# Performance work log

Measured on AMD Instinct MI355X. Metric: run time of the kernel, lower is better.

The kernel has to match this reference:

```python
import jax, jax.numpy as jnp
import numpy as np

N_NODES = 50000
N_EDGES = 800000
IN_DIM = 256
OUT_DIM = 32
HEADS = 4
NEG_SLOPE = 0.2  # PyG GATConv default
LN_EPS = 1e-5


def setup_inputs() -> dict:
    key = jax.random.key(0)
    ks = jax.random.split(key, 8)
    x = jax.random.normal(ks[0], (N_NODES, IN_DIM), dtype=jnp.float32)
    edge_index = jax.random.randint(ks[1], (2, N_EDGES), 0, N_NODES, dtype=jnp.int64)
    # Glorot-ish scaling for stability
    W = jax.random.normal(ks[2], (IN_DIM, HEADS * OUT_DIM), dtype=jnp.float32) / np.sqrt(IN_DIM)
    att_src = jax.random.normal(ks[3], (HEADS, OUT_DIM), dtype=jnp.float32) / np.sqrt(OUT_DIM)
    att_dst = jax.random.normal(ks[4], (HEADS, OUT_DIM), dtype=jnp.float32) / np.sqrt(OUT_DIM)
    bias = jax.random.normal(ks[5], (HEADS * OUT_DIM,), dtype=jnp.float32) * 0.02
    gamma = jnp.ones((HEADS * OUT_DIM,), dtype=jnp.float32)
    beta = jnp.zeros((HEADS * OUT_DIM,), dtype=jnp.float32)
    return {"x": x, "edge_index": edge_index, "W": W, "att_src": att_src,
            "att_dst": att_dst, "bias": bias, "gamma": gamma, "beta": beta}


def reference(x, edge_index, W, att_src, att_dst, bias, gamma, beta):
    N = x.shape[0]
    H, C = att_src.shape
    # --- GATConv (PyG semantics, eval mode so attention dropout is identity) ---
    # add self-loops (PyG default add_self_loops=True)
    loops = jnp.arange(N, dtype=edge_index.dtype)
    src = jnp.concatenate([edge_index[0], loops])  # [E+N]
    dst = jnp.concatenate([edge_index[1], loops])
    h = (x @ W).reshape(N, H, C)                    # [N,H,C] (lin has no bias)
    a_s = jnp.einsum('nhc,hc->nh', h, att_src)      # [N,H]
    a_d = jnp.einsum('nhc,hc->nh', h, att_dst)
    e = jax.nn.leaky_relu(a_s[src] + a_d[dst], NEG_SLOPE)  # [E+N,H]
    # segment softmax over incoming edges of each destination node
    emax = jax.ops.segment_max(e, dst, num_segments=N)     # every node has a self-loop
    ee = jnp.exp(e - emax[dst])
    denom = jax.ops.segment_sum(ee, dst, num_segments=N)
    alpha = ee / denom[dst]                                 # [E+N,H]
    msg = h[src] * alpha[:, :, None]                        # [E+N,H,C]
    out = jax.ops.segment_sum(msg, dst, num_segments=N).reshape(N, H * C) + bias
    # --- LayerNorm ---
    mu = out.mean(-1, keepdims=True)
    var = ((out - mu) ** 2).mean(-1, keepdims=True)
    out = (out - mu) * jax.lax.rsqrt(var + LN_EPS) * gamma + beta
    # --- dropout (eval: identity) + ELU ---
    return jax.nn.elu(out)
```

## Files before the change

kernel.cpp:

```cpp
#include <hip/hip_runtime.h>
#include <hip/hip_bf16.h>
#include <cstdint>
#include <cstddef>

#define N_NODES 50000
#define N_EDGES 800000
#define IN_DIM 256
#define HC 128
#define HEADS 4
#define NEG_SLOPE 0.2f
#define LN_EPS 1e-5f

#define POISON_I ((int)0xAAAAAAAAu)

#define NSB ((N_NODES + 255) / 256)

typedef _Float16 f16x8 __attribute__((ext_vector_type(8)));
typedef _Float16 f16x2 __attribute__((ext_vector_type(2)));
typedef float f32x4 __attribute__((ext_vector_type(4)));

__device__ __forceinline__ float lrelu(float x) { return x > 0.f ? x : NEG_SLOPE * x; }
__device__ __forceinline__ unsigned pack_h2(float a, float b) {
    f16x2 h; h[0] = (_Float16)a; h[1] = (_Float16)b;
    return *(unsigned*)&h;
}

__global__ __launch_bounds__(256) void k_histW(
    const int* __restrict__ ei, const float* __restrict__ W,
    _Float16* __restrict__ W16, int* __restrict__ counts,
    int* __restrict__ rank)
{
    int b = blockIdx.x;
    if (b < 16) {
        int c = b * 256 + threadIdx.x;
        int col = c & 15, quad = (c >> 4) & 3, nt = (c >> 6) & 7, kt = c >> 9;
        int n = nt * 16 + col;
        f16x8 v;
#pragma unroll
        for (int j = 0; j < 8; ++j) {
            int k = kt * 32 + quad * 8 + j;
            v[j] = (_Float16)W[k * HC + n];
        }
        *(f16x8*)(W16 + (size_t)c * 8) = v;
    } else {
        int e = (b - 16) * 256 + threadIdx.x;
        if (e < N_EDGES)
            rank[e] = atomicAdd(&counts[ei[N_EDGES + e]], 1) - POISON_I;
    }
}

__global__ __launch_bounds__(256) void k1_mfma(
    const float* __restrict__ x, const _Float16* __restrict__ W16,
    const float* __restrict__ att_src, const float* __restrict__ att_dst,
    _Float16* __restrict__ h16, float* __restrict__ a_s, float* __restrict__ a_d)
{
    __shared__ _Float16 Wlds[32768];
    const int tid = threadIdx.x;

    {
        const uint4* g4 = (const uint4*)W16;
        uint4* s4 = (uint4*)Wlds;
#pragma unroll
        for (int it = 0; it < 16; ++it) s4[it * 256 + tid] = g4[it * 256 + tid];
    }

    const int wave = tid >> 6;
    const int lane = tid & 63;
    const int col  = lane & 15;
    const int quad = lane >> 4;
    const int m0   = blockIdx.x * 64 + wave * 16;

    const int rowA = min(m0 + col, N_NODES - 1);
    const float* xrow = x + (size_t)rowA * IN_DIM + quad * 8;

    float4 xr[16];
#pragma unroll
    for (int kt = 0; kt < 8; ++kt) {
        xr[2 * kt]     = *(const float4*)(xrow + kt * 32);
        xr[2 * kt + 1] = *(const float4*)(xrow + kt * 32 + 4);
    }
    __syncthreads();

    f32x4 acc[8];
#pragma unroll
    for (int nt = 0; nt < 8; ++nt) acc[nt] = (f32x4){0.f, 0.f, 0.f, 0.f};

#pragma unroll
    for (int kt = 0; kt < 8; ++kt) {
        float4 xa = xr[2 * kt], xb = xr[2 * kt + 1];
        f16x8 a;
        a[0] = (_Float16)xa.x; a[1] = (_Float16)xa.y;
        a[2] = (_Float16)xa.z; a[3] = (_Float16)xa.w;
        a[4] = (_Float16)xb.x; a[5] = (_Float16)xb.y;
        a[6] = (_Float16)xb.z; a[7] = (_Float16)xb.w;
#pragma unroll
        for (int nt = 0; nt < 8; ++nt) {
            f16x8 b = *(const f16x8*)&Wlds[((kt * 8 + nt) * 64 + quad * 16 + col) * 8];
            acc[nt] = __builtin_amdgcn_mfma_f32_16x16x32_f16(a, b, acc[nt], 0, 0, 0);
        }
    }

    f16x2* h2g = (f16x2*)h16;
#pragma unroll
    for (int a2 = 0; a2 < 4; ++a2) {
#pragma unroll
        for (int r = 0; r < 4; ++r) {
            int row = m0 + quad * 4 + r;
            if (row < N_NODES) {
                f16x2 hv;
                hv[0] = (_Float16)acc[2 * a2][r];
                hv[1] = (_Float16)acc[2 * a2 + 1][r];
                h2g[(size_t)row * 64 + a2 * 16 + col] = hv;
            }
        }
    }

    float pS[4][4], pD[4][4];
#pragma unroll
    for (int hd = 0; hd < 4; ++hd)
#pragma unroll
        for (int r = 0; r < 4; ++r) { pS[hd][r] = 0.f; pD[hd][r] = 0.f; }

#pragma unroll
    for (int nt = 0; nt < 8; ++nt) {
        int ch = nt * 16 + col;
        float sv = att_src[ch], dv = att_dst[ch];
        int hd = nt >> 1;
#pragma unroll
        for (int r = 0; r < 4; ++r) {
            pS[hd][r] += acc[nt][r] * sv;
            pD[hd][r] += acc[nt][r] * dv;
        }
    }
#pragma unroll
    for (int off = 1; off < 16; off <<= 1) {
#pragma unroll
        for (int hd = 0; hd < 4; ++hd)
#pragma unroll
            for (int r = 0; r < 4; ++r) {
                pS[hd][r] += __shfl_xor(pS[hd][r], off, 16);
                pD[hd][r] += __shfl_xor(pD[hd][r], off, 16);
            }
    }
    if (col == 0) {
#pragma unroll
        for (int r = 0; r < 4; ++r) {
            int row = m0 + quad * 4 + r;
            if (row < N_NODES) {
#pragma unroll
                for (int hd = 0; hd < 4; ++hd) {
                    a_s[row * HEADS + hd] = pS[hd][r];
                    a_d[row * HEADS + hd] = pD[hd][r];
                }
            }
        }
    }
}

__global__ __launch_bounds__(256) void k_scan1(const int* __restrict__ counts,
                                               int* __restrict__ starts,
                                               int* __restrict__ bsum) {
    __shared__ int s[256];
    int i = blockIdx.x * 256 + threadIdx.x;
    int v = (i < N_NODES) ? (counts[i] - POISON_I) : 0;
    s[threadIdx.x] = v; __syncthreads();
#pragma unroll
    for (int off = 1; off < 256; off <<= 1) {
        int t = (threadIdx.x >= off) ? s[threadIdx.x - off] : 0;
        __syncthreads();
        s[threadIdx.x] += t;
        __syncthreads();
    }
    if (i < N_NODES) starts[i] = s[threadIdx.x] - v;
    if (threadIdx.x == 255) bsum[blockIdx.x] = s[255];
}
__global__ __launch_bounds__(256) void k_scan2(int* __restrict__ bsum, int nb) {
    __shared__ int s[256];
    int v = (threadIdx.x < nb) ? bsum[threadIdx.x] : 0;
    s[threadIdx.x] = v; __syncthreads();
#pragma unroll
    for (int off = 1; off < 256; off <<= 1) {
        int t = (threadIdx.x >= off) ? s[threadIdx.x - off] : 0;
        __syncthreads();
        s[threadIdx.x] += t;
        __syncthreads();
    }
    if (threadIdx.x < nb) bsum[threadIdx.x] = s[threadIdx.x] - v;
}

__global__ __launch_bounds__(256) void k_scatter(
    const int* __restrict__ ei, const int* __restrict__ starts,
    const int* __restrict__ bsum, const int* __restrict__ rank,
    const float* __restrict__ a_s, const float* __restrict__ a_d,
    int4* __restrict__ rec)
{
    int e = blockIdx.x * 256 + threadIdx.x;
    if (e >= N_EDGES) return;
    int src = ei[e], dst = ei[N_EDGES + e];
    float4 s4 = *(const float4*)(a_s + (size_t)src * HEADS);
    float4 d4 = *(const float4*)(a_d + (size_t)dst * HEADS);
    float w0 = __expf(lrelu(s4.x + d4.x));
    float w1 = __expf(lrelu(s4.y + d4.y));
    float w2 = __expf(lrelu(s4.z + d4.z));
    float w3 = __expf(lrelu(s4.w + d4.w));
    int p = starts[dst] + bsum[dst >> 8] + rank[e];
    int4 r;
    r.x = src;
    r.y = (int)pack_h2(w0, w1);
    r.z = (int)pack_h2(w2, w3);
    r.w = 0;
    rec[p] = r;
}

__global__ __launch_bounds__(256) void k_gather(
    const int* __restrict__ starts, const int* __restrict__ bsum,
    const int* __restrict__ counts, const int4* __restrict__ rec,
    const float* __restrict__ a_s, const float* __restrict__ a_d,
    const _Float16* __restrict__ h16, const float* __restrict__ bias,
    const float* __restrict__ gamma, const float* __restrict__ beta,
    float* __restrict__ out)
{
    __shared__ int   lsrc[256];
    __shared__ uint2 lw[256];

    int gid = blockIdx.x * 256 + threadIdx.x;
    int n = gid >> 6, lane = gid & 63;
    if (n >= N_NODES) return;

    const int wbase = (threadIdx.x >> 6) * 64;
    const int beg = starts[n] + bsum[n >> 8];
    const int deg = counts[n] - POISON_I;
    const int hd = lane >> 4;
    const f16x2* h2 = (const f16x2*)h16;
    const unsigned short* lwh = (const unsigned short*)&lw[wbase];

    const float wSelf = __expf(lrelu(a_s[n * HEADS + hd] + a_d[n * HEADS + hd]));
    float den = wSelf;
    f16x2 hv = h2[(size_t)n * 64 + lane];
    float acc0 = (float)hv[0] * wSelf;
    float acc1 = (float)hv[1] * wSelf;

    for (int base = 0; base < deg; base += 64) {
        int nc = min(64, deg - base);
        if (lane < nc) {
            int4 rv = rec[beg + base + lane];
            lsrc[wbase + lane] = rv.x;
            lw[wbase + lane] = (uint2){(unsigned)rv.y, (unsigned)rv.z};
        }
        int j = 0;
        for (; j + 8 <= nc; j += 8) {
            int s[8]; float w[8]; f16x2 hh[8];
#pragma unroll
            for (int k = 0; k < 8; ++k) {
                s[k] = lsrc[wbase + j + k];
                unsigned short uw = lwh[(j + k) * 4 + hd];
                _Float16 wf = *(_Float16*)&uw;
                w[k] = (float)wf;
            }
#pragma unroll
            for (int k = 0; k < 8; ++k) hh[k] = h2[(size_t)s[k] * 64 + lane];
#pragma unroll
            for (int k = 0; k < 8; ++k) {
                acc0 += (float)hh[k][0] * w[k];
                acc1 += (float)hh[k][1] * w[k];
                den  += w[k];
            }
        }
        for (; j < nc; ++j) {
            int s0 = lsrc[wbase + j];
            unsigned short uw = lwh[j * 4 + hd];
            _Float16 wf = *(_Float16*)&uw;
            float w0 = (float)wf;
            f16x2 hx = h2[(size_t)s0 * 64 + lane];
            acc0 += (float)hx[0] * w0;
            acc1 += (float)hx[1] * w0;
            den  += w0;
        }
    }

    const int c0 = (lane >> 4) * 32 + (lane & 15);
    const int c1 = c0 + 16;
    float v0 = acc0 / den + bias[c0];
    float v1 = acc1 / den + bias[c1];
    float s = v0 + v1;
#pragma unroll
    for (int off = 32; off; off >>= 1) s += __shfl_xor(s, off, 64);
    float mu = s * (1.f / 128.f);
    float d0 = v0 - mu, d1 = v1 - mu;
    float q = d0 * d0 + d1 * d1;
#pragma unroll
    for (int off = 32; off; off >>= 1) q += __shfl_xor(q, off, 64);
    float rs = rsqrtf(q * (1.f / 128.f) + LN_EPS);
    float o0 = d0 * rs * gamma[c0] + beta[c0];
    float o1 = d1 * rs * gamma[c1] + beta[c1];
    o0 = o0 > 0.f ? o0 : __expf(o0) - 1.f;
    o1 = o1 > 0.f ? o1 : __expf(o1) - 1.f;
    out[(size_t)n * HC + c0] = o0;
    out[(size_t)n * HC + c1] = o1;
}

extern "C" void kernel_launch(void* const* d_in, const int* in_sizes, int n_in,
                              void* d_out, int out_size, void* d_ws, size_t ws_size,
                              hipStream_t stream) {
    const float* x       = (const float*)d_in[0];
    const int*   ei      = (const int*)d_in[1];
    const float* W       = (const float*)d_in[2];
    const float* att_src = (const float*)d_in[3];
    const float* att_dst = (const float*)d_in[4];
    const float* bias    = (const float*)d_in[5];
    const float* gamma   = (const float*)d_in[6];
    const float* beta    = (const float*)d_in[7];
    float* out = (float*)d_out;

    char* ws = (char*)d_ws;
    _Float16* h16    = (_Float16*)(ws);
    float*    a_s    = (float*)(ws + 12800000);
    float*    a_d    = (float*)(ws + 13600000);
    int4*     rec    = (int4*) (ws + 14400000);
    int*      rank   = (int*)  (ws + 27200000);
    int*      counts = (int*)  (ws + 30400000);
    int*      starts = (int*)  (ws + 30600000);
    int*      bsum   = (int*)  (ws + 30800000);
    _Float16* W16    = (_Float16*)(ws + 30810240);

    k_histW<<<16 + (N_EDGES + 255) / 256, 256, 0, stream>>>(ei, W, W16, counts,
                                                            rank);
    k1_mfma<<<(N_NODES + 63) / 64, 256, 0, stream>>>(x, W16, att_src, att_dst,
                                                     h16, a_s, a_d);
    k_scan1<<<NSB, 256, 0, stream>>>(counts, starts, bsum);
    k_scan2<<<1, 256, 0, stream>>>(bsum, NSB);
    k_scatter<<<(N_EDGES + 255) / 256, 256, 0, stream>>>(ei, starts, bsum, rank,
                                                         a_s, a_d, rec);
    k_gather<<<(N_NODES * 64 + 255) / 256, 256, 0, stream>>>(
        starts, bsum, counts, rec, a_s, a_d, h16, bias, gamma, beta, out);
}
```

Measured before the change: 209.2 us.

## Compute attention weights in gather instead of scatter, store only sorted src

The scatter kernel now writes only the source index (4 bytes) per edge into CSR order instead of a 16-byte record carrying fp16 exp weights. The gather kernel loads a_s for each neighbour and computes the leaky-relu/exp weights itself, keeping them in fp32 shared memory. This cuts scatter write traffic and the record read in gather, and removes the fp16 rounding of the weights. In exchange, gather does an extra random 16-byte a_s load and four exps per edge, and its shared memory use grows.

```diff
diff --git a/kernel.cpp b/kernel.cpp
--- a/kernel.cpp
+++ b/kernel.cpp
@@ -20,10 +20,6 @@
 typedef float f32x4 __attribute__((ext_vector_type(4)));
 
 __device__ __forceinline__ float lrelu(float x) { return x > 0.f ? x : NEG_SLOPE * x; }
-__device__ __forceinline__ unsigned pack_h2(float a, float b) {
-    f16x2 h; h[0] = (_Float16)a; h[1] = (_Float16)b;
-    return *(unsigned*)&h;
-}
 
 __global__ __launch_bounds__(256) void k_histW(
     const int* __restrict__ ei, const float* __restrict__ W,
@@ -191,37 +187,25 @@
 __global__ __launch_bounds__(256) void k_scatter(
     const int* __restrict__ ei, const int* __restrict__ starts,
     const int* __restrict__ bsum, const int* __restrict__ rank,
-    const float* __restrict__ a_s, const float* __restrict__ a_d,
-    int4* __restrict__ rec)
+    int* __restrict__ ssrc)
 {
     int e = blockIdx.x * 256 + threadIdx.x;
     if (e >= N_EDGES) return;
     int src = ei[e], dst = ei[N_EDGES + e];
-    float4 s4 = *(const float4*)(a_s + (size_t)src * HEADS);
-    float4 d4 = *(const float4*)(a_d + (size_t)dst * HEADS);
-    float w0 = __expf(lrelu(s4.x + d4.x));
-    float w1 = __expf(lrelu(s4.y + d4.y));
-    float w2 = __expf(lrelu(s4.z + d4.z));
-    float w3 = __expf(lrelu(s4.w + d4.w));
     int p = starts[dst] + bsum[dst >> 8] + rank[e];
-    int4 r;
-    r.x = src;
-    r.y = (int)pack_h2(w0, w1);
-    r.z = (int)pack_h2(w2, w3);
-    r.w = 0;
-    rec[p] = r;
+    ssrc[p] = src;
 }
 
 __global__ __launch_bounds__(256) void k_gather(
     const int* __restrict__ starts, const int* __restrict__ bsum,
-    const int* __restrict__ counts, const int4* __restrict__ rec,
+    const int* __restrict__ counts, const int* __restrict__ ssrc,
     const float* __restrict__ a_s, const float* __restrict__ a_d,
     const _Float16* __restrict__ h16, const float* __restrict__ bias,
     const float* __restrict__ gamma, const float* __restrict__ beta,
     float* __restrict__ out)
 {
     __shared__ int   lsrc[256];
-    __shared__ uint2 lw[256];
+    __shared__ float lws[256 * 4];
 
     int gid = blockIdx.x * 256 + threadIdx.x;
     int n = gid >> 6, lane = gid & 63;
@@ -232,9 +216,12 @@
     const int deg = counts[n] - POISON_I;
     const int hd = lane >> 4;
     const f16x2* h2 = (const f16x2*)h16;
-    const unsigned short* lwh = (const unsigned short*)&lw[wbase];
-
-    const float wSelf = __expf(lrelu(a_s[n * HEADS + hd] + a_d[n * HEADS + hd]));
+
+    float4 d4 = *(const float4*)(a_d + (size_t)n * HEADS);
+    const float adH = (hd & 2) ? ((hd & 1) ? d4.w : d4.z)
+                               : ((hd & 1) ? d4.y : d4.x);
+
+    const float wSelf = __expf(lrelu(a_s[n * HEADS + hd] + adH));
     float den = wSelf;
     f16x2 hv = h2[(size_t)n * 64 + lane];
     float acc0 = (float)hv[0] * wSelf;
@@ -243,9 +230,14 @@
     for (int base = 0; base < deg; base += 64) {
         int nc = min(64, deg - base);
         if (lane < nc) {
-            int4 rv = rec[beg + base + lane];
-            lsrc[wbase + lane] = rv.x;
-            lw[wbase + lane] = (uint2){(unsigned)rv.y, (unsigned)rv.z};
+            int src = ssrc[beg + base + lane];
+            lsrc[wbase + lane] = src;
+            float4 s4 = *(const float4*)(a_s + (size_t)src * HEADS);
+            float* q = &lws[(wbase + lane) * 4];
+            q[0] = __expf(lrelu(s4.x + d4.x));
+            q[1] = __expf(lrelu(s4.y + d4.y));
+            q[2] = __expf(lrelu(s4.z + d4.z));
+            q[3] = __expf(lrelu(s4.w + d4.w));
         }
         int j = 0;
         for (; j + 8 <= nc; j += 8) {
@@ -253,9 +245,7 @@
 #pragma unroll
             for (int k = 0; k < 8; ++k) {
                 s[k] = lsrc[wbase + j + k];
-                unsigned short uw = lwh[(j + k) * 4 + hd];
-                _Float16 wf = *(_Float16*)&uw;
-                w[k] = (float)wf;
+                w[k] = lws[(wbase + j + k) * 4 + hd];
             }
 #pragma unroll
             for (int k = 0; k < 8; ++k) hh[k] = h2[(size_t)s[k] * 64 + lane];
@@ -268,9 +258,7 @@
         }
         for (; j < nc; ++j) {
             int s0 = lsrc[wbase + j];
-            unsigned short uw = lwh[j * 4 + hd];
-            _Float16 wf = *(_Float16*)&uw;
-            float w0 = (float)wf;
+            float w0 = lws[(wbase + j) * 4 + hd];
             f16x2 hx = h2[(size_t)s0 * 64 + lane];
             acc0 += (float)hx[0] * w0;
             acc1 += (float)hx[1] * w0;
@@ -316,8 +304,8 @@
     _Float16* h16    = (_Float16*)(ws);
     float*    a_s    = (float*)(ws + 12800000);
     float*    a_d    = (float*)(ws + 13600000);
-    int4*     rec    = (int4*) (ws + 14400000);
-    int*      rank   = (int*)  (ws + 27200000);
+    int*      ssrc   = (int*)  (ws + 14400000);
+    int*      rank   = (int*)  (ws + 17600000);
     int*      counts = (int*)  (ws + 30400000);
     int*      starts = (int*)  (ws + 30600000);
     int*      bsum   = (int*)  (ws + 30800000);
@@ -330,7 +318,7 @@
     k_scan1<<<NSB, 256, 0, stream>>>(counts, starts, bsum);
     k_scan2<<<1, 256, 0, stream>>>(bsum, NSB);
     k_scatter<<<(N_EDGES + 255) / 256, 256, 0, stream>>>(ei, starts, bsum, rank,
-                                                         a_s, a_d, rec);
+                                                         ssrc);
     k_gather<<<(N_NODES * 64 + 255) / 256, 256, 0, stream>>>(
-        starts, bsum, counts, rec, a_s, a_d, h16, bias, gamma, beta, out);
-}
+        starts, bsum, counts, ssrc, a_s, a_d, h16, bias, gamma, beta, out);
+}
```

Result: no change. 211.3 us (+1.0%).
